# Performance work log

Hardware: AMD Instinct MI355X
Metric: run time of the kernel (lower is better)

## Reference

```python
import jax, jax.numpy as jnp
import numpy as np

N_NODES = 50000
N_EDGES = 800000
IN_DIM = 768
HIDDEN = 256
N_CLASSES = 10
N_GRAPHS = 128


def setup_inputs() -> dict:
    key = jax.random.key(0)
    ks = jax.random.split(key, 10)
    emb = jax.random.normal(ks[0], (N_NODES, IN_DIM), dtype=jnp.float32)
    edge_index = jax.random.randint(ks[1], (2, N_EDGES), 0, N_NODES, dtype=jnp.int32)
    batch = jnp.sort(jax.random.randint(ks[2], (N_NODES,), 0, N_GRAPHS, dtype=jnp.int32))
    # GCNConv weights (glorot-ish scale) and biases
    W1 = jax.random.normal(ks[3], (IN_DIM, HIDDEN), dtype=jnp.float32) / np.sqrt(IN_DIM)
    b1 = jnp.zeros((HIDDEN,), dtype=jnp.float32)
    W2 = jax.random.normal(ks[4], (HIDDEN, HIDDEN), dtype=jnp.float32) / np.sqrt(HIDDEN)
    b2 = jnp.zeros((HIDDEN,), dtype=jnp.float32)
    Wfc = jax.random.normal(ks[5], (HIDDEN, N_CLASSES), dtype=jnp.float32) / np.sqrt(HIDDEN)
    bfc = jnp.zeros((N_CLASSES,), dtype=jnp.float32)
    return {"emb": emb, "edge_index": edge_index, "batch": batch,
            "W1": W1, "b1": b1, "W2": W2, "b2": b2, "Wfc": Wfc, "bfc": bfc}


def _gcn_conv(x, src, dst, W, b, n_nodes):
    # PyG GCNConv: x' = D^{-1/2} (A + I) D^{-1/2} X W + b, self-loops included
    h = x @ W                                   # [N, H] dense GEMM
    deg = jax.ops.segment_sum(jnp.ones_like(dst, dtype=h.dtype), dst,
                              num_segments=n_nodes)
    dinv = jnp.where(deg > 0, jax.lax.rsqrt(deg), 0.0)
    norm = dinv[src] * dinv[dst]                # [E+N]
    msgs = h[src] * norm[:, None]               # gather [E+N, H]
    out = jax.ops.segment_sum(msgs, dst, num_segments=n_nodes)  # scatter-add
    return out + b


def reference(emb, edge_index, batch, W1, b1, W2, b2, Wfc, bfc):
    n_nodes = emb.shape[0]
    loops = jnp.arange(n_nodes, dtype=edge_index.dtype)
    src = jnp.concatenate([edge_index[0], loops])  # add self-loops
    dst = jnp.concatenate([edge_index[1], loops])

    x = jax.nn.relu(_gcn_conv(emb, src, dst, W1, b1, n_nodes))
    # F.dropout(p=0.3) is a no-op in eval mode (training=False)
    x = _gcn_conv(x, src, dst, W2, b2, n_nodes)

    # global_mean_pool over graph ids
    sums = jax.ops.segment_sum(x, batch, num_segments=N_GRAPHS)
    cnts = jax.ops.segment_sum(jnp.ones((n_nodes,), dtype=x.dtype), batch,
                               num_segments=N_GRAPHS)
    pooled = sums / jnp.maximum(cnts, 1.0)[:, None]  # [G, H]
    return pooled @ Wfc + bfc                        # [G, C]
```

## Files before the change

kernel.cpp:

```cpp
#include <hip/hip_runtime.h>

#define N_NODES 50000
#define N_EDGES 800000
#define IN_DIM 768
#define HIDDEN 256
#define N_CLASSES 10
#define N_GRAPHS 128

typedef __attribute__((ext_vector_type(8))) short bf16x8;
typedef __attribute__((ext_vector_type(4))) float f32x4;
typedef __attribute__((ext_vector_type(8))) unsigned short u16x8;

__device__ __forceinline__ float bf2f(unsigned short u) {
    union { unsigned int i; float f; } c; c.i = ((unsigned int)u) << 16; return c.f;
}
__device__ __forceinline__ unsigned short f2bf(float f) {
    unsigned int x = __float_as_uint(f);
    return (unsigned short)((x + 0x7fffu + ((x >> 16) & 1u)) >> 16);
}

__device__ __forceinline__ void gload16(const void* g, void* l) {
    __builtin_amdgcn_global_load_lds((const __attribute__((address_space(1))) void*)g,
                                     (__attribute__((address_space(3))) void*)l, 16, 0, 0);
}

__global__ void zero_int(int* p, int n) {
    int i = blockIdx.x * blockDim.x + threadIdx.x;
    if (i < n) p[i] = 0;
}

__global__ void zero_f32(float* p, int n) {
    int i = blockIdx.x * blockDim.x + threadIdx.x;
    if (i < n) p[i] = 0.f;
}

__global__ void hist_dst(const int* __restrict__ dst, int* __restrict__ cnt) {
    int e = blockIdx.x * blockDim.x + threadIdx.x;
    if (e < N_EDGES) atomicAdd(&cnt[dst[e]], 1);
}

__global__ __launch_bounds__(1024) void scan_kernel(const int* __restrict__ cnt,
                                                    int* __restrict__ rowstart,
                                                    int* __restrict__ cursor,
                                                    float* __restrict__ dinv) {
    __shared__ int wsum[16];
    __shared__ int chunk_carry;
    const int tid = threadIdx.x, lane = tid & 63, wid = tid >> 6;
    if (tid == 0) chunk_carry = 0;
    __syncthreads();
    for (int base = 0; base < N_NODES; base += 1024) {
        int i = base + tid;
        int v = (i < N_NODES) ? cnt[i] : 0;
        if (i < N_NODES) dinv[i] = rsqrtf(1.0f + (float)v);
        int s = v;
#pragma unroll
        for (int d = 1; d < 64; d <<= 1) { int t = __shfl_up(s, d); if (lane >= d) s += t; }
        if (lane == 63) wsum[wid] = s;
        __syncthreads();
        if (tid < 16) {
            int ww = wsum[tid];
#pragma unroll
            for (int d = 1; d < 16; d <<= 1) { int t = __shfl_up(ww, d); if (tid >= d) ww += t; }
            wsum[tid] = ww;
        }
        __syncthreads();
        int wpre = (wid == 0) ? 0 : wsum[wid - 1];
        int excl = chunk_carry + wpre + s - v;
        if (i < N_NODES) { rowstart[i] = excl; cursor[i] = excl; }
        int total = wsum[15];
        __syncthreads();
        if (tid == 0) chunk_carry += total;
        __syncthreads();
    }
    if (threadIdx.x == 0) rowstart[N_NODES] = chunk_carry;
}

__global__ void scatter_edges(const int* __restrict__ src, const int* __restrict__ dst,
                              int* __restrict__ cursor, int* __restrict__ col) {
    int e = blockIdx.x * blockDim.x + threadIdx.x;
    if (e >= N_EDGES) return;
    int d = dst[e];
    int pos = atomicAdd(&cursor[d], 1);
    col[pos] = src[e];
}

__global__ __launch_bounds__(256) void transpose_w_bf16(const float* __restrict__ W,
                                                        unsigned short* __restrict__ WT, int K) {
    __shared__ float t[32][33];
    int tx = threadIdx.x & 31, ty = threadIdx.x >> 5;
    int k0 = blockIdx.x * 32, n0 = blockIdx.y * 32;
#pragma unroll
    for (int i = 0; i < 4; ++i) {
        int k = k0 + ty + i * 8;
        t[ty + i * 8][tx] = W[(size_t)k * 256 + n0 + tx];
    }
    __syncthreads();
#pragma unroll
    for (int i = 0; i < 4; ++i) {
        int n = n0 + ty + i * 8;
        WT[(size_t)n * K + k0 + tx] = f2bf(t[tx][ty + i * 8]);
    }
}

template <int K, bool CVT>
__global__ __launch_bounds__(256, 2) void gemm_mfma(const void* __restrict__ Av,
                                                    const unsigned short* __restrict__ BT,
                                                    unsigned short* __restrict__ C, int M) {
    constexpr int NS = K / 64;
    __shared__ uint4 sm[5120];
    uint4* As = sm;
    uint4* Bs = sm + 1024;
    const int tid = threadIdx.x;
    const int lane = tid & 63, w = tid >> 6;
    const int lr = lane & 15, kg = lane >> 4;
    const int bm = blockIdx.x * 64;

    const int ra = tid >> 2;
    const int ca = (tid & 3) * 2;
    int rga = bm + ra; rga = rga < M ? rga : M - 1;

    f32x4 acc[16] = {};

    {
        if constexpr (CVT) {
            const float* p = &((const float*)Av)[(size_t)rga * K + ca * 8];
            float4 u0 = ((const float4*)p)[0], u1 = ((const float4*)p)[1];
            float4 u2 = ((const float4*)p)[2], u3 = ((const float4*)p)[3];
            u16x8 o0, o1;
            o0[0] = f2bf(u0.x); o0[1] = f2bf(u0.y); o0[2] = f2bf(u0.z); o0[3] = f2bf(u0.w);
            o0[4] = f2bf(u1.x); o0[5] = f2bf(u1.y); o0[6] = f2bf(u1.z); o0[7] = f2bf(u1.w);
            o1[0] = f2bf(u2.x); o1[1] = f2bf(u2.y); o1[2] = f2bf(u2.z); o1[3] = f2bf(u2.w);
            o1[4] = f2bf(u3.x); o1[5] = f2bf(u3.y); o1[6] = f2bf(u3.z); o1[7] = f2bf(u3.w);
            *(u16x8*)&As[ra * 8 + (ca ^ (ra & 7))] = o0;
            *(u16x8*)&As[ra * 8 + ((ca + 1) ^ (ra & 7))] = o1;
        } else {
            const unsigned short* Ab = (const unsigned short*)Av;
            uint4 v0 = *(const uint4*)&Ab[(size_t)rga * K + ca * 8];
            uint4 v1 = *(const uint4*)&Ab[(size_t)rga * K + ca * 8 + 8];
            As[ra * 8 + (ca ^ (ra & 7))] = v0;
            As[ra * 8 + ((ca + 1) ^ (ra & 7))] = v1;
        }
#pragma unroll
        for (int i = 0; i < 8; ++i) {
            int glin = w * 512 + i * 64 + lane;
            int n = glin >> 3, g = glin & 7;
            int gs = g ^ (n & 7);
            gload16(&BT[(size_t)n * K + gs * 8], &Bs[w * 512 + i * 64]);
        }
    }
    __syncthreads();

    for (int k = 0; k < NS; ++k) {
        const int cur = k & 1, nxt = cur ^ 1;
        const int kk1 = (k + 1) * 64;
        float4 u0, u1, u2, u3;
        uint4 v0, v1;
        if (k + 1 < NS) {
#pragma unroll
            for (int i = 0; i < 8; ++i) {
                int glin = w * 512 + i * 64 + lane;
                int n = glin >> 3, g = glin & 7;
                int gs = g ^ (n & 7);
                gload16(&BT[(size_t)n * K + kk1 + gs * 8], &Bs[nxt * 2048 + w * 512 + i * 64]);
            }
            if constexpr (CVT) {
                const float* p = &((const float*)Av)[(size_t)rga * K + kk1 + ca * 8];
                u0 = ((const float4*)p)[0]; u1 = ((const float4*)p)[1];
                u2 = ((const float4*)p)[2]; u3 = ((const float4*)p)[3];
            } else {
                const unsigned short* Ab = (const unsigned short*)Av;
                v0 = *(const uint4*)&Ab[(size_t)rga * K + kk1 + ca * 8];
                v1 = *(const uint4*)&Ab[(size_t)rga * K + kk1 + ca * 8 + 8];
            }
        }
#pragma unroll
        for (int h = 0; h < 2; ++h) {
            int r0 = 16 * w + lr;
            int gc = 4 * h + kg;
            bf16x8 a0 = *(const bf16x8*)&As[cur * 512 + r0 * 8 + (gc ^ (r0 & 7))];
#pragma unroll
            for (int f = 0; f < 16; ++f) {
                int nr = 16 * f + lr;
                bf16x8 bf = *(const bf16x8*)&Bs[cur * 2048 + nr * 8 + (gc ^ (nr & 7))];
                acc[f] = __builtin_amdgcn_mfma_f32_16x16x32_bf16(bf, a0, acc[f], 0, 0, 0);
            }
        }
        if (k + 1 < NS) {
            if constexpr (CVT) {
                u16x8 o0, o1;
                o0[0] = f2bf(u0.x); o0[1] = f2bf(u0.y); o0[2] = f2bf(u0.z); o0[3] = f2bf(u0.w);
                o0[4] = f2bf(u1.x); o0[5] = f2bf(u1.y); o0[6] = f2bf(u1.z); o0[7] = f2bf(u1.w);
                o1[0] = f2bf(u2.x); o1[1] = f2bf(u2.y); o1[2] = f2bf(u2.z); o1[3] = f2bf(u2.w);
                o1[4] = f2bf(u3.x); o1[5] = f2bf(u3.y); o1[6] = f2bf(u3.z); o1[7] = f2bf(u3.w);
                *(u16x8*)&As[nxt * 512 + ra * 8 + (ca ^ (ra & 7))] = o0;
                *(u16x8*)&As[nxt * 512 + ra * 8 + ((ca + 1) ^ (ra & 7))] = o1;
            } else {
                As[nxt * 512 + ra * 8 + (ca ^ (ra & 7))] = v0;
                As[nxt * 512 + ra * 8 + ((ca + 1) ^ (ra & 7))] = v1;
            }
        }
        __syncthreads();
    }

    int orow = bm + 16 * w + lr;
    if (orow < M) {
#pragma unroll
        for (int f = 0; f < 16; ++f) {
            ushort4 o = make_ushort4(f2bf(acc[f][0]), f2bf(acc[f][1]),
                                     f2bf(acc[f][2]), f2bf(acc[f][3]));
            *(ushort4*)&C[(size_t)orow * 256 + 16 * f + 4 * kg] = o;
        }
    }
}

template <bool RELU, bool OUTBF>
__global__ __launch_bounds__(256) void agg_csr(const unsigned short* __restrict__ h,
                                               const float* __restrict__ dinv,
                                               const int* __restrict__ rowstart,
                                               const int* __restrict__ col,
                                               const float* __restrict__ bias,
                                               void* __restrict__ outv) {
    int node = (blockIdx.x * 256 + threadIdx.x) >> 6;
    if (node >= N_NODES) return;
    const int lane = threadIdx.x & 63;
    const int half = lane >> 5, sl = lane & 31;

    float dd = dinv[node];
    float acc[8] = {};

    {
        u16x8 hv = *(const u16x8*)&h[(size_t)node * 256 + sl * 8];
        float wgt = half ? 0.f : dd * dd;
#pragma unroll
        for (int i = 0; i < 8; ++i) acc[i] += bf2f(hv[i]) * wgt;
    }

    int j0 = rowstart[node], jend = rowstart[node + 1];
    int j = j0;
    for (; j + 8 <= jend; j += 8) {
        int s0 = col[j + half];
        int s1 = col[j + 2 + half];
        int s2 = col[j + 4 + half];
        int s3 = col[j + 6 + half];
        float n0 = dinv[s0] * dd, n1 = dinv[s1] * dd;
        float n2 = dinv[s2] * dd, n3 = dinv[s3] * dd;
        u16x8 v0 = *(const u16x8*)&h[(size_t)s0 * 256 + sl * 8];
        u16x8 v1 = *(const u16x8*)&h[(size_t)s1 * 256 + sl * 8];
        u16x8 v2 = *(const u16x8*)&h[(size_t)s2 * 256 + sl * 8];
        u16x8 v3 = *(const u16x8*)&h[(size_t)s3 * 256 + sl * 8];
#pragma unroll
        for (int i = 0; i < 8; ++i)
            acc[i] += bf2f(v0[i]) * n0 + bf2f(v1[i]) * n1 + bf2f(v2[i]) * n2 + bf2f(v3[i]) * n3;
    }
    for (; j < jend; j += 2) {
        int sidx = j + half;
        bool p = sidx < jend;
        int s = p ? col[sidx] : node;
        float nrm = p ? dinv[s] * dd : 0.f;
        u16x8 v = *(const u16x8*)&h[(size_t)s * 256 + sl * 8];
#pragma unroll
        for (int i = 0; i < 8; ++i) acc[i] += bf2f(v[i]) * nrm;
    }

#pragma unroll
    for (int i = 0; i < 8; ++i) acc[i] += __shfl_xor(acc[i], 32);

    if (half == 0) {
        float4 b0 = *(const float4*)&bias[sl * 8];
        float4 b1 = *(const float4*)&bias[sl * 8 + 4];
        acc[0] += b0.x; acc[1] += b0.y; acc[2] += b0.z; acc[3] += b0.w;
        acc[4] += b1.x; acc[5] += b1.y; acc[6] += b1.z; acc[7] += b1.w;
        if (RELU) {
#pragma unroll
            for (int i = 0; i < 8; ++i) acc[i] = fmaxf(acc[i], 0.f);
        }
        if (OUTBF) {
            u16x8 o;
#pragma unroll
            for (int i = 0; i < 8; ++i) o[i] = f2bf(acc[i]);
            *(u16x8*)((unsigned short*)outv + (size_t)node * 256 + sl * 8) = o;
        } else {
            float* ob = (float*)outv + (size_t)node * 256 + sl * 8;
            *(float4*)ob = make_float4(acc[0], acc[1], acc[2], acc[3]);
            *(float4*)(ob + 4) = make_float4(acc[4], acc[5], acc[6], acc[7]);
        }
    }
}

#define POOL_CHUNK 49
__global__ __launch_bounds__(256) void pool_partial(const float* __restrict__ x,
                                                    const int* __restrict__ batch,
                                                    float* __restrict__ gsum) {
    int lo = blockIdx.x * POOL_CHUNK;
    if (lo >= N_NODES) return;
    int hi = lo + POOL_CHUNK; if (hi > N_NODES) hi = N_NODES;
    int c = threadIdx.x;
    int g = batch[lo];
    float acc = 0.f;
    for (int n = lo; n < hi; ++n) {
        int gn = batch[n];
        if (gn != g) { atomicAdd(&gsum[g * 256 + c], acc); acc = 0.f; g = gn; }
        acc += x[(size_t)n * 256 + c];
    }
    atomicAdd(&gsum[g * 256 + c], acc);
}

__global__ __launch_bounds__(256) void fc_head(const float* __restrict__ gsum,
                                               const int* __restrict__ batch,
                                               const float* __restrict__ Wfc,
                                               const float* __restrict__ bfc,
                                               float* __restrict__ out) {
    int g = blockIdx.x;
    int c = threadIdx.x;
    int lo = 0, hi = N_NODES;
    while (lo < hi) { int m = (lo + hi) >> 1; if (batch[m] < g) lo = m + 1; else hi = m; }
    int lo2 = lo, hi2 = N_NODES;
    while (lo2 < hi2) { int m = (lo2 + hi2) >> 1; if (batch[m] < g + 1) lo2 = m + 1; else hi2 = m; }
    float inv = 1.0f / fmaxf((float)(lo2 - lo), 1.0f);
    __shared__ float pooled[256];
    pooled[c] = gsum[(size_t)g * 256 + c] * inv;
    __syncthreads();
    if (c < N_CLASSES) {
        float acc = bfc[c];
        for (int k = 0; k < 256; ++k) acc += pooled[k] * Wfc[k * N_CLASSES + c];
        out[g * N_CLASSES + c] = acc;
    }
}

extern "C" void kernel_launch(void* const* d_in, const int* in_sizes, int n_in,
                              void* d_out, int out_size, void* d_ws, size_t ws_size,
                              hipStream_t stream) {
    const float* emb  = (const float*)d_in[0];
    const int*   eidx = (const int*)d_in[1];
    const int*   batch= (const int*)d_in[2];
    const float* W1   = (const float*)d_in[3];
    const float* b1   = (const float*)d_in[4];
    const float* W2   = (const float*)d_in[5];
    const float* b2   = (const float*)d_in[6];
    const float* Wfc  = (const float*)d_in[7];
    const float* bfc  = (const float*)d_in[8];
    float* out = (float*)d_out;

    const int* src = eidx;
    const int* dst = eidx + N_EDGES;

    char* ws = (char*)d_ws;
    size_t off = 0;
    auto alloc = [&](size_t bytes) { void* p = ws + off; off += (bytes + 1023) & ~(size_t)1023; return p; };
    int*   rowcnt   = (int*)alloc(N_NODES * 4);
    int*   rowstart = (int*)alloc((N_NODES + 1) * 4);
    int*   cursor   = (int*)alloc(N_NODES * 4);
    int*   col      = (int*)alloc(N_EDGES * 4);
    float* dinv     = (float*)alloc(N_NODES * 4);
    float* gsum     = (float*)alloc((size_t)N_GRAPHS * 256 * 4);
    unsigned short* W1T = (unsigned short*)alloc((size_t)HIDDEN * IN_DIM * 2);
    unsigned short* W2T = (unsigned short*)alloc((size_t)HIDDEN * HIDDEN * 2);
    unsigned short* bufH = (unsigned short*)alloc((size_t)N_NODES * 256 * 2);
    unsigned short* x1 = (unsigned short*)alloc((size_t)N_NODES * 256 * 2);
    float* x2 = (float*)alloc((size_t)N_NODES * 256 * 4);

    const int NB = (N_NODES + 255) / 256;
    const int EBk = (N_EDGES + 255) / 256;
    const int AGG_B = (N_NODES * 64 + 255) / 256;
    dim3 gemm_grid((N_NODES + 63) / 64, 1);
    const int POOL_B = (N_NODES + POOL_CHUNK - 1) / POOL_CHUNK;

    zero_int<<<NB, 256, 0, stream>>>(rowcnt, N_NODES);
    hist_dst<<<EBk, 256, 0, stream>>>(dst, rowcnt);
    scan_kernel<<<1, 1024, 0, stream>>>(rowcnt, rowstart, cursor, dinv);
    scatter_edges<<<EBk, 256, 0, stream>>>(src, dst, cursor, col);
    zero_f32<<<(N_GRAPHS * 256 + 255) / 256, 256, 0, stream>>>(gsum, N_GRAPHS * 256);

    transpose_w_bf16<<<dim3(IN_DIM / 32, 8), 256, 0, stream>>>(W1, W1T, IN_DIM);
    transpose_w_bf16<<<dim3(HIDDEN / 32, 8), 256, 0, stream>>>(W2, W2T, HIDDEN);

    gemm_mfma<IN_DIM, true><<<gemm_grid, 256, 0, stream>>>(emb, W1T, bufH, N_NODES);
    agg_csr<true, true><<<AGG_B, 256, 0, stream>>>(bufH, dinv, rowstart, col, b1, x1);

    gemm_mfma<HIDDEN, false><<<gemm_grid, 256, 0, stream>>>(x1, W2T, bufH, N_NODES);
    agg_csr<false, false><<<AGG_B, 256, 0, stream>>>(bufH, dinv, rowstart, col, b2, x2);

    pool_partial<<<POOL_B, 256, 0, stream>>>(x2, batch, gsum);
    fc_head<<<N_GRAPHS, 256, 0, stream>>>(gsum, batch, Wfc, bfc, out);
}
```

Before: 396.4 us.

## Fold second GCN layer through mean pooling to skip second GEMM and aggregation

Uses linearity of the second GCN layer and the mean pool: it pools the normalized adjacency applied to x1 per graph, then applies W2, b2 and the FC head on only 128 pooled rows. This removes the second dense GEMM, the second neighbor aggregation and the large fp32 x2 buffer. Per-edge normalization and graph ids are precomputed during CSR construction so the first aggregation and the new edge-pool kernel read them directly. The edge pooling adds float atomics at graph boundaries and changes the summation order.

```diff
diff --git a/kernel.cpp b/kernel.cpp
--- a/kernel.cpp
+++ b/kernel.cpp
@@ -76,12 +76,16 @@
 }
 
 __global__ void scatter_edges(const int* __restrict__ src, const int* __restrict__ dst,
-                              int* __restrict__ cursor, int* __restrict__ col) {
+                              const int* __restrict__ batch, const float* __restrict__ dinv,
+                              int* __restrict__ cursor, int* __restrict__ col,
+                              float* __restrict__ nrm, int* __restrict__ gid) {
     int e = blockIdx.x * blockDim.x + threadIdx.x;
     if (e >= N_EDGES) return;
-    int d = dst[e];
+    int s = src[e], d = dst[e];
     int pos = atomicAdd(&cursor[d], 1);
-    col[pos] = src[e];
+    col[pos] = s;
+    nrm[pos] = dinv[s] * dinv[d];
+    gid[pos] = batch[d];
 }
 
 __global__ __launch_bounds__(256) void transpose_w_bf16(const float* __restrict__ W,
@@ -218,6 +222,7 @@
                                                const float* __restrict__ dinv,
                                                const int* __restrict__ rowstart,
                                                const int* __restrict__ col,
+                                               const float* __restrict__ nrm,
                                                const float* __restrict__ bias,
                                                void* __restrict__ outv) {
     int node = (blockIdx.x * 256 + threadIdx.x) >> 6;
@@ -242,8 +247,8 @@
         int s1 = col[j + 2 + half];
         int s2 = col[j + 4 + half];
         int s3 = col[j + 6 + half];
-        float n0 = dinv[s0] * dd, n1 = dinv[s1] * dd;
-        float n2 = dinv[s2] * dd, n3 = dinv[s3] * dd;
+        float n0 = nrm[j + half], n1 = nrm[j + 2 + half];
+        float n2 = nrm[j + 4 + half], n3 = nrm[j + 6 + half];
         u16x8 v0 = *(const u16x8*)&h[(size_t)s0 * 256 + sl * 8];
         u16x8 v1 = *(const u16x8*)&h[(size_t)s1 * 256 + sl * 8];
         u16x8 v2 = *(const u16x8*)&h[(size_t)s2 * 256 + sl * 8];
@@ -255,11 +260,12 @@
     for (; j < jend; j += 2) {
         int sidx = j + half;
         bool p = sidx < jend;
-        int s = p ? col[sidx] : node;
-        float nrm = p ? dinv[s] * dd : 0.f;
+        int si = p ? sidx : (jend - 1);
+        int s = col[si];
+        float w = p ? nrm[si] : 0.f;
         u16x8 v = *(const u16x8*)&h[(size_t)s * 256 + sl * 8];
 #pragma unroll
-        for (int i = 0; i < 8; ++i) acc[i] += bf2f(v[i]) * nrm;
+        for (int i = 0; i < 8; ++i) acc[i] += bf2f(v[i]) * w;
     }
 
 #pragma unroll
@@ -288,9 +294,10 @@
 }
 
 #define POOL_CHUNK 49
-__global__ __launch_bounds__(256) void pool_partial(const float* __restrict__ x,
-                                                    const int* __restrict__ batch,
-                                                    float* __restrict__ gsum) {
+__global__ __launch_bounds__(256) void pool_self(const unsigned short* __restrict__ x1,
+                                                 const int* __restrict__ batch,
+                                                 const float* __restrict__ dinv,
+                                                 float* __restrict__ P) {
     int lo = blockIdx.x * POOL_CHUNK;
     if (lo >= N_NODES) return;
     int hi = lo + POOL_CHUNK; if (hi > N_NODES) hi = N_NODES;
@@ -299,17 +306,77 @@
     float acc = 0.f;
     for (int n = lo; n < hi; ++n) {
         int gn = batch[n];
-        if (gn != g) { atomicAdd(&gsum[g * 256 + c], acc); acc = 0.f; g = gn; }
-        acc += x[(size_t)n * 256 + c];
-    }
-    atomicAdd(&gsum[g * 256 + c], acc);
-}
-
-__global__ __launch_bounds__(256) void fc_head(const float* __restrict__ gsum,
-                                               const int* __restrict__ batch,
-                                               const float* __restrict__ Wfc,
-                                               const float* __restrict__ bfc,
-                                               float* __restrict__ out) {
+        if (gn != g) { atomicAdd(&P[g * 256 + c], acc); acc = 0.f; g = gn; }
+        float w = dinv[n]; w *= w;
+        acc += bf2f(x1[(size_t)n * 256 + c]) * w;
+    }
+    atomicAdd(&P[g * 256 + c], acc);
+}
+
+#define PE_BLOCKS 2048
+__global__ __launch_bounds__(256) void pool_edge(const unsigned short* __restrict__ x1,
+                                                 const int* __restrict__ col,
+                                                 const float* __restrict__ nrm,
+                                                 const int* __restrict__ gid,
+                                                 float* __restrict__ P) {
+    int wv = (blockIdx.x * 256 + threadIdx.x) >> 6;
+    const int lane = threadIdx.x & 63;
+    const int NW = PE_BLOCKS * 4;
+    const int per = (N_EDGES + NW - 1) / NW;
+    int j0 = wv * per, j1 = j0 + per;
+    if (j1 > N_EDGES) j1 = N_EDGES;
+    if (j0 >= j1) return;
+
+    float a0 = 0.f, a1 = 0.f, a2 = 0.f, a3 = 0.f;
+    int gcur = gid[j0];
+
+    if (gid[j1 - 1] == gcur) {
+        int j = j0;
+        for (; j + 2 <= j1; j += 2) {
+            int s0 = col[j], s1 = col[j + 1];
+            float w0 = nrm[j], w1 = nrm[j + 1];
+            ushort4 v0 = *(const ushort4*)&x1[(size_t)s0 * 256 + lane * 4];
+            ushort4 v1 = *(const ushort4*)&x1[(size_t)s1 * 256 + lane * 4];
+            a0 += bf2f(v0.x) * w0 + bf2f(v1.x) * w1;
+            a1 += bf2f(v0.y) * w0 + bf2f(v1.y) * w1;
+            a2 += bf2f(v0.z) * w0 + bf2f(v1.z) * w1;
+            a3 += bf2f(v0.w) * w0 + bf2f(v1.w) * w1;
+        }
+        if (j < j1) {
+            int s = col[j]; float w = nrm[j];
+            ushort4 v = *(const ushort4*)&x1[(size_t)s * 256 + lane * 4];
+            a0 += bf2f(v.x) * w; a1 += bf2f(v.y) * w;
+            a2 += bf2f(v.z) * w; a3 += bf2f(v.w) * w;
+        }
+    } else {
+        for (int j = j0; j < j1; ++j) {
+            int g = gid[j];
+            if (g != gcur) {
+                atomicAdd(&P[gcur * 256 + lane * 4 + 0], a0);
+                atomicAdd(&P[gcur * 256 + lane * 4 + 1], a1);
+                atomicAdd(&P[gcur * 256 + lane * 4 + 2], a2);
+                atomicAdd(&P[gcur * 256 + lane * 4 + 3], a3);
+                a0 = a1 = a2 = a3 = 0.f; gcur = g;
+            }
+            int s = col[j]; float w = nrm[j];
+            ushort4 v = *(const ushort4*)&x1[(size_t)s * 256 + lane * 4];
+            a0 += bf2f(v.x) * w; a1 += bf2f(v.y) * w;
+            a2 += bf2f(v.z) * w; a3 += bf2f(v.w) * w;
+        }
+    }
+    atomicAdd(&P[gcur * 256 + lane * 4 + 0], a0);
+    atomicAdd(&P[gcur * 256 + lane * 4 + 1], a1);
+    atomicAdd(&P[gcur * 256 + lane * 4 + 2], a2);
+    atomicAdd(&P[gcur * 256 + lane * 4 + 3], a3);
+}
+
+__global__ __launch_bounds__(256) void head(const float* __restrict__ P,
+                                            const int* __restrict__ batch,
+                                            const float* __restrict__ W2,
+                                            const float* __restrict__ b2,
+                                            const float* __restrict__ Wfc,
+                                            const float* __restrict__ bfc,
+                                            float* __restrict__ out) {
     int g = blockIdx.x;
     int c = threadIdx.x;
     int lo = 0, hi = N_NODES;
@@ -317,13 +384,19 @@
     int lo2 = lo, hi2 = N_NODES;
     while (lo2 < hi2) { int m = (lo2 + hi2) >> 1; if (batch[m] < g + 1) lo2 = m + 1; else hi2 = m; }
     float inv = 1.0f / fmaxf((float)(lo2 - lo), 1.0f);
-    __shared__ float pooled[256];
-    pooled[c] = gsum[(size_t)g * 256 + c] * inv;
+
+    __shared__ float pp[256];
+    __shared__ float zz[256];
+    pp[c] = P[(size_t)g * 256 + c] * inv;
+    __syncthreads();
+    float z = b2[c];
+    for (int k = 0; k < 256; ++k) z += pp[k] * W2[(size_t)k * 256 + c];
+    zz[c] = z;
     __syncthreads();
     if (c < N_CLASSES) {
-        float acc = bfc[c];
-        for (int k = 0; k < 256; ++k) acc += pooled[k] * Wfc[k * N_CLASSES + c];
-        out[g * N_CLASSES + c] = acc;
+        float o = bfc[c];
+        for (int k = 0; k < 256; ++k) o += zz[k] * Wfc[k * N_CLASSES + c];
+        out[g * N_CLASSES + c] = o;
     }
 }
 
@@ -351,13 +424,13 @@
     int*   rowstart = (int*)alloc((N_NODES + 1) * 4);
     int*   cursor   = (int*)alloc(N_NODES * 4);
     int*   col      = (int*)alloc(N_EDGES * 4);
+    float* nrm      = (float*)alloc(N_EDGES * 4);
+    int*   gid      = (int*)alloc(N_EDGES * 4);
     float* dinv     = (float*)alloc(N_NODES * 4);
-    float* gsum     = (float*)alloc((size_t)N_GRAPHS * 256 * 4);
+    float* P        = (float*)alloc((size_t)N_GRAPHS * 256 * 4);
     unsigned short* W1T = (unsigned short*)alloc((size_t)HIDDEN * IN_DIM * 2);
-    unsigned short* W2T = (unsigned short*)alloc((size_t)HIDDEN * HIDDEN * 2);
     unsigned short* bufH = (unsigned short*)alloc((size_t)N_NODES * 256 * 2);
     unsigned short* x1 = (unsigned short*)alloc((size_t)N_NODES * 256 * 2);
-    float* x2 = (float*)alloc((size_t)N_NODES * 256 * 4);
 
     const int NB = (N_NODES + 255) / 256;
     const int EBk = (N_EDGES + 255) / 256;
@@ -368,18 +441,16 @@
     zero_int<<<NB, 256, 0, stream>>>(rowcnt, N_NODES);
     hist_dst<<<EBk, 256, 0, stream>>>(dst, rowcnt);
     scan_kernel<<<1, 1024, 0, stream>>>(rowcnt, rowstart, cursor, dinv);
-    scatter_edges<<<EBk, 256, 0, stream>>>(src, dst, cursor, col);
-    zero_f32<<<(N_GRAPHS * 256 + 255) / 256, 256, 0, stream>>>(gsum, N_GRAPHS * 256);
+    scatter_edges<<<EBk, 256, 0, stream>>>(src, dst, batch, dinv, cursor, col, nrm, gid);
+    zero_f32<<<(N_GRAPHS * 256 + 255) / 256, 256, 0, stream>>>(P, N_GRAPHS * 256);
 
     transpose_w_bf16<<<dim3(IN_DIM / 32, 8), 256, 0, stream>>>(W1, W1T, IN_DIM);
-    transpose_w_bf16<<<dim3(HIDDEN / 32, 8), 256, 0, stream>>>(W2, W2T, HIDDEN);
 
     gemm_mfma<IN_DIM, true><<<gemm_grid, 256, 0, stream>>>(emb, W1T, bufH, N_NODES);
-    agg_csr<true, true><<<AGG_B, 256, 0, stream>>>(bufH, dinv, rowstart, col, b1, x1);
-
-    gemm_mfma<HIDDEN, false><<<gemm_grid, 256, 0, stream>>>(x1, W2T, bufH, N_NODES);
-    agg_csr<false, false><<<AGG_B, 256, 0, stream>>>(bufH, dinv, rowstart, col, b2, x2);
-
-    pool_partial<<<POOL_B, 256, 0, stream>>>(x2, batch, gsum);
-    fc_head<<<N_GRAPHS, 256, 0, stream>>>(gsum, batch, Wfc, bfc, out);
-}
+    agg_csr<true, true><<<AGG_B, 256, 0, stream>>>(bufH, dinv, rowstart, col, nrm, b1, x1);
+
+    pool_self<<<POOL_B, 256, 0, stream>>>(x1, batch, dinv, P);
+    pool_edge<<<PE_BLOCKS, 256, 0, stream>>>(x1, col, nrm, gid, P);
+
+    head<<<N_GRAPHS, 256, 0, stream>>>(P, batch, W2, b2, Wfc, bfc, out);
+}
```

New measurement: 407.7 us. 1.03x slower.
